# Optimization experiments

Hardware: AMD Instinct MI355X
Metric: run time of the kernel (lower is better)

Reference implementation:

```python
import jax, jax.numpy as jnp
import numpy as np

NUM_NODES = 50000
NUM_EDGES = 600000
NUM_FEAT = 128
HIDDEN = 512
N_OUT = 128
K = 3
N_GRAPHS = 128


def setup_inputs() -> dict:
    key = jax.random.key(0)
    ks = jax.random.split(key, 12)
    feature = jax.random.normal(ks[0], (NUM_NODES, NUM_FEAT), dtype=jnp.float32)
    edge_index = jax.random.randint(ks[1], (2, NUM_EDGES), 0, NUM_NODES, dtype=jnp.int64)
    protein_batch = jnp.sort(jax.random.randint(ks[2], (NUM_NODES,), 0, N_GRAPHS, dtype=jnp.int64))
    s = 0.05
    # ChebConv weights stored [K, in, out] (x @ W), single shared bias per conv
    W1 = jax.random.normal(ks[3], (K, NUM_FEAT, NUM_FEAT), dtype=jnp.float32) * s
    b1 = jax.random.normal(ks[4], (NUM_FEAT,), dtype=jnp.float32) * s
    W2 = jax.random.normal(ks[5], (K, NUM_FEAT, 2 * NUM_FEAT), dtype=jnp.float32) * s
    b2 = jax.random.normal(ks[6], (2 * NUM_FEAT,), dtype=jnp.float32) * s
    fc1_w = jax.random.normal(ks[7], (3 * NUM_FEAT, HIDDEN), dtype=jnp.float32) * s
    fc1_b = jax.random.normal(ks[8], (HIDDEN,), dtype=jnp.float32) * s
    fc2_w = jax.random.normal(ks[9], (HIDDEN, N_OUT), dtype=jnp.float32) * s
    fc2_b = jax.random.normal(ks[10], (N_OUT,), dtype=jnp.float32) * s
    return {"feature": feature, "edge_index": edge_index, "protein_batch": protein_batch,
            "W1": W1, "b1": b1, "W2": W2, "b2": b2,
            "fc1_w": fc1_w, "fc1_b": fc1_b, "fc2_w": fc2_w, "fc2_b": fc2_b}


def _cheb_conv(x, src, dst, edge_w, W, b):
    # PyG ChebConv with sym normalization, lambda_max=2 => scaled Laplacian
    # L_hat has zero diagonal and off-diag weights -1/sqrt(d_i d_j) (edge_w).
    def prop(h):
        return jax.ops.segment_sum(edge_w[:, None] * h[src], dst, num_segments=NUM_NODES)

    Tx0 = x
    out = Tx0 @ W[0]
    Tx1 = prop(x)
    out = out + Tx1 @ W[1]
    for k in range(2, W.shape[0]):
        Tx2 = 2.0 * prop(Tx1) - Tx0
        out = out + Tx2 @ W[k]
        Tx0, Tx1 = Tx1, Tx2
    return out + b


def reference(feature, edge_index, protein_batch, W1, b1, W2, b2, fc1_w, fc1_b, fc2_w, fc2_b):
    src, dst = edge_index[0], edge_index[1]
    deg = jax.ops.segment_sum(jnp.ones_like(src, dtype=feature.dtype), src, num_segments=NUM_NODES)
    dinv = jnp.where(deg > 0, jax.lax.rsqrt(jnp.maximum(deg, 1.0)), 0.0)
    edge_w = -dinv[src] * dinv[dst]  # (2/lambda_max)*L_sym off-diagonal; diag cancels to 0

    gx = jax.nn.relu(_cheb_conv(feature, src, dst, edge_w, W1, b1))
    gx = jax.nn.relu(_cheb_conv(gx, src, dst, edge_w, W2, b2))
    gx = jnp.concatenate([gx, feature], axis=1)  # [N, 3*F]

    # global_mean_pool
    sums = jax.ops.segment_sum(gx, protein_batch, num_segments=N_GRAPHS)
    cnts = jax.ops.segment_sum(jnp.ones((gx.shape[0],), gx.dtype), protein_batch, num_segments=N_GRAPHS)
    pooled = sums / jnp.maximum(cnts, 1.0)[:, None]

    h = jax.nn.relu(pooled @ fc1_w + fc1_b)  # dropout is identity in eval
    return h @ fc2_w + fc2_b
```

## Files before the change

kernel.cpp:

```cpp
#include <hip/hip_runtime.h>
#include <hip/hip_bf16.h>

#define NNODES 50000
#define NEDGES 600000
#define NB 196

typedef short vs8 __attribute__((ext_vector_type(8)));
typedef float floatx4 __attribute__((ext_vector_type(4)));

__device__ __forceinline__ float us2f(unsigned short u) {
    unsigned int x = ((unsigned int)u) << 16;
    float f;
    __builtin_memcpy(&f, &x, 4);
    return f;
}
__device__ __forceinline__ unsigned short f2us(float f) {
    unsigned int x;
    __builtin_memcpy(&x, &f, 4);
    unsigned int r = x + 0x7fffu + ((x >> 16) & 1u);
    return (unsigned short)(r >> 16);
}
__device__ __forceinline__ float ldf(const void* p, int i, int ff) {
    if (ff) return us2f(((const unsigned short*)p)[i]);
    return ((const float*)p)[i];
}
__device__ __forceinline__ int2 ldnt_sw(const int2* p) {
    unsigned long long v =
        __builtin_nontemporal_load(reinterpret_cast<const unsigned long long*>(p));
    int2 r;
    r.x = (int)(unsigned int)(v & 0xffffffffULL);
    r.y = (int)(unsigned int)(v >> 32);
    return r;
}

__global__ void k_detect(const int* ei, const unsigned int* fw, int* iflag, int* fflag) {
    int lane = threadIdx.x;
    int odd1 = ei[2 * lane + 1];
    int odd2 = ei[128 + 2 * lane + 1];
    unsigned long long nz = __ballot(odd1 != 0 || odd2 != 0);
    unsigned int e = (fw[lane] >> 7) & 0xffu;
    unsigned long long h = __ballot(e > 100u && e < 160u);
    if (lane == 0) {
        *iflag = (nz == 0ULL) ? 1 : 0;
        *fflag = (__popcll(h) > 40) ? 1 : 0;
    }
}

__global__ void k_init(const int* pb, const int* iflag, int* deg, int* indeg,
                       int* b32, float* psum) {
    int i = blockIdx.x * 256 + threadIdx.x;
    if (i < NNODES) {
        deg[i] = 0;
        indeg[i] = 0;
        int f = *iflag;
        b32[i] = pb[((size_t)i) << f];
    }
    if (i < 128 * 384) psum[i] = 0.f;
}

__global__ void k_degree(const int* ei, const int* iflag, int* deg, int* indeg,
                         int* rank) {
    int e = blockIdx.x * blockDim.x + threadIdx.x;
    if (e >= NEDGES) return;
    int f = *iflag;
    int s = ei[((size_t)e) << f];
    int d = ei[((size_t)(NEDGES + e)) << f];
    atomicAdd(&deg[s], 1);
    int r = atomicAdd(&indeg[d], 1);
    rank[e] = r;
}

__global__ void k_scan1(const int* indeg, const int* deg, int* bsum, float* dinv) {
    __shared__ int sh[256];
    int t = threadIdx.x;
    int i = blockIdx.x * 256 + t;
    int v = (i < NNODES) ? indeg[i] : 0;
    if (i < NNODES) {
        int d = deg[i];
        dinv[i] = d > 0 ? rsqrtf((float)d) : 0.f;
    }
    sh[t] = v;
    __syncthreads();
    for (int off = 128; off > 0; off >>= 1) {
        if (t < off) sh[t] += sh[t + off];
        __syncthreads();
    }
    if (t == 0) bsum[blockIdx.x] = sh[0];
}

__global__ void k_scan2(const int* bsum, int* boff, int* rowptr,
                        const int* batch32, int* pcnt) {
    __shared__ int sh[256];
    int t = threadIdx.x;
    int v = (t < NB) ? bsum[t] : 0;
    sh[t] = v;
    __syncthreads();
    for (int off = 1; off < 256; off <<= 1) {
        int x = (t >= off) ? sh[t - off] : 0;
        __syncthreads();
        sh[t] += x;
        __syncthreads();
    }
    if (t < NB) boff[t] = sh[t] - v;
    if (t == 255) rowptr[NNODES] = sh[255];
    if (t < 128) {
        int g = t;
        int lo = 0, hi = NNODES;
        while (lo < hi) { int mid = (lo + hi) >> 1; if (batch32[mid] < g) lo = mid + 1; else hi = mid; }
        int start = lo;
        hi = NNODES;
        while (lo < hi) { int mid = (lo + hi) >> 1; if (batch32[mid] <= g) lo = mid + 1; else hi = mid; }
        pcnt[g] = lo - start;
    }
}

__global__ void k_scan3(const int* indeg, const int* boff, int* rowptr) {
    __shared__ int sh[256];
    int t = threadIdx.x;
    int i = blockIdx.x * 256 + t;
    int v = (i < NNODES) ? indeg[i] : 0;
    sh[t] = v;
    __syncthreads();
    for (int off = 1; off < 256; off <<= 1) {
        int x = (t >= off) ? sh[t - off] : 0;
        __syncthreads();
        sh[t] += x;
        __syncthreads();
    }
    int excl = sh[t] - v + boff[blockIdx.x];
    if (i < NNODES) rowptr[i] = excl;
}

__global__ void k_fill(const int* ei, const int* iflag, const float* dinv,
                       const int* rowptr, const int* rank, int2* csr_sw) {
    int e = blockIdx.x * blockDim.x + threadIdx.x;
    if (e >= NEDGES) return;
    int f = *iflag;
    int s = ei[((size_t)e) << f];
    int d = ei[((size_t)(NEDGES + e)) << f];
    float w = -dinv[s] * dinv[d];
    int p = rowptr[d] + rank[e];
    int wb;
    __builtin_memcpy(&wb, &w, 4);
    int2 sw;
    sw.x = s;
    sw.y = wb;
    csr_sw[p] = sw;
}

__global__ void k_featb(const void* src, const int* fflag, unsigned short* dst) {
    int i = blockIdx.x * 256 + threadIdx.x;
    if (i >= NNODES * 128 / 8) return;
    if (*fflag) {
        reinterpret_cast<uint4*>(dst)[i] = reinterpret_cast<const uint4*>(src)[i];
    } else {
        const float4* fs = reinterpret_cast<const float4*>(src);
        float4 a = fs[2 * i], b = fs[2 * i + 1];
        uint4 o;
        o.x = (unsigned int)f2us(a.x) | ((unsigned int)f2us(a.y) << 16);
        o.y = (unsigned int)f2us(a.z) | ((unsigned int)f2us(a.w) << 16);
        o.z = (unsigned int)f2us(b.x) | ((unsigned int)f2us(b.y) << 16);
        o.w = (unsigned int)f2us(b.z) | ((unsigned int)f2us(b.w) << 16);
        reinterpret_cast<uint4*>(dst)[i] = o;
    }
}

__global__ void k_trans2(const void* W1, const void* W2, const int* fflag,
                         unsigned short* W1t, unsigned short* W2t) {
    int idx = blockIdx.x * 256 + threadIdx.x;
    int ff = *fflag;
    if (idx < 49152) {
        int n = idx / 384, k = idx - n * 384;
        float v;
        if (k < 128) v = ldf(W1, k * 128 + n, ff) - ldf(W1, (256 + k) * 128 + n, ff);
        else if (k < 256) v = ldf(W1, k * 128 + n, ff);
        else v = 2.f * ldf(W1, k * 128 + n, ff);
        W1t[idx] = f2us(v);
    } else if (idx < 49152 + 98304) {
        int j = idx - 49152;
        int n = j / 384, k = j - n * 384;
        float v;
        if (k < 128) v = ldf(W2, k * 256 + n, ff) - ldf(W2, (256 + k) * 256 + n, ff);
        else if (k < 256) v = ldf(W2, k * 256 + n, ff);
        else v = 2.f * ldf(W2, k * 256 + n, ff);
        W2t[j] = f2us(v);
    }
}

__global__ void k_prepw(const void* b1, const void* b2, const void* f1w, const void* f1b,
                        const void* f2w, const void* f2b, const int* fflag,
                        float* b1f, float* b2f, float* f1wf, float* f1bf,
                        float* f2wf, float* f2bf) {
    int i = blockIdx.x * 256 + threadIdx.x;
    int ff = *fflag;
    if (i < 196608) { f1wf[i] = ldf(f1w, i, ff); return; }
    i -= 196608;
    if (i < 65536) { f2wf[i] = ldf(f2w, i, ff); return; }
    i -= 65536;
    if (i < 512) { f1bf[i] = ldf(f1b, i, ff); return; }
    i -= 512;
    if (i < 256) { b2f[i] = ldf(b2, i, ff); return; }
    i -= 256;
    if (i < 128) { b1f[i] = ldf(b1, i, ff); return; }
    i -= 128;
    if (i < 128) f2bf[i] = ldf(f2b, i, ff);
}

__global__ void k_prop(const unsigned short* X, const int* rowptr, const int2* csr_sw,
                       unsigned short* out) {
    int wvid = (blockIdx.x * blockDim.x + threadIdx.x) >> 6;
    int lane = threadIdx.x & 63;
    int q = lane >> 4;
    int ln = lane & 15;
    int node = wvid * 4 + q;
    if (node >= NNODES) return;
    int fo = ln * 8;
    int beg = rowptr[node], end = rowptr[node + 1];
    float a0 = 0.f, a1 = 0.f, a2 = 0.f, a3 = 0.f;
    float a4 = 0.f, a5 = 0.f, a6 = 0.f, a7 = 0.f;
    int j = beg;
    for (; j + 4 <= end; j += 4) {
        int2 e0 = ldnt_sw(csr_sw + j);
        int2 e1 = ldnt_sw(csr_sw + j + 1);
        int2 e2 = ldnt_sw(csr_sw + j + 2);
        int2 e3 = ldnt_sw(csr_sw + j + 3);
        uint4 u0 = *reinterpret_cast<const uint4*>(X + (size_t)e0.x * 128 + fo);
        uint4 u1 = *reinterpret_cast<const uint4*>(X + (size_t)e1.x * 128 + fo);
        uint4 u2 = *reinterpret_cast<const uint4*>(X + (size_t)e2.x * 128 + fo);
        uint4 u3 = *reinterpret_cast<const uint4*>(X + (size_t)e3.x * 128 + fo);
        float w0, w1, w2, w3;
        __builtin_memcpy(&w0, &e0.y, 4);
        __builtin_memcpy(&w1, &e1.y, 4);
        __builtin_memcpy(&w2, &e2.y, 4);
        __builtin_memcpy(&w3, &e3.y, 4);
        a0 += w0 * us2f((unsigned short)(u0.x & 0xffffu)) + w1 * us2f((unsigned short)(u1.x & 0xffffu))
            + w2 * us2f((unsigned short)(u2.x & 0xffffu)) + w3 * us2f((unsigned short)(u3.x & 0xffffu));
        a1 += w0 * us2f((unsigned short)(u0.x >> 16)) + w1 * us2f((unsigned short)(u1.x >> 16))
            + w2 * us2f((unsigned short)(u2.x >> 16)) + w3 * us2f((unsigned short)(u3.x >> 16));
        a2 += w0 * us2f((unsigned short)(u0.y & 0xffffu)) + w1 * us2f((unsigned short)(u1.y & 0xffffu))
            + w2 * us2f((unsigned short)(u2.y & 0xffffu)) + w3 * us2f((unsigned short)(u3.y & 0xffffu));
        a3 += w0 * us2f((unsigned short)(u0.y >> 16)) + w1 * us2f((unsigned short)(u1.y >> 16))
            + w2 * us2f((unsigned short)(u2.y >> 16)) + w3 * us2f((unsigned short)(u3.y >> 16));
        a4 += w0 * us2f((unsigned short)(u0.z & 0xffffu)) + w1 * us2f((unsigned short)(u1.z & 0xffffu))
            + w2 * us2f((unsigned short)(u2.z & 0xffffu)) + w3 * us2f((unsigned short)(u3.z & 0xffffu));
        a5 += w0 * us2f((unsigned short)(u0.z >> 16)) + w1 * us2f((unsigned short)(u1.z >> 16))
            + w2 * us2f((unsigned short)(u2.z >> 16)) + w3 * us2f((unsigned short)(u3.z >> 16));
        a6 += w0 * us2f((unsigned short)(u0.w & 0xffffu)) + w1 * us2f((unsigned short)(u1.w & 0xffffu))
            + w2 * us2f((unsigned short)(u2.w & 0xffffu)) + w3 * us2f((unsigned short)(u3.w & 0xffffu));
        a7 += w0 * us2f((unsigned short)(u0.w >> 16)) + w1 * us2f((unsigned short)(u1.w >> 16))
            + w2 * us2f((unsigned short)(u2.w >> 16)) + w3 * us2f((unsigned short)(u3.w >> 16));
    }
    for (; j < end; ++j) {
        int2 e = ldnt_sw(csr_sw + j);
        float w;
        __builtin_memcpy(&w, &e.y, 4);
        uint4 u = *reinterpret_cast<const uint4*>(X + (size_t)e.x * 128 + fo);
        a0 += w * us2f((unsigned short)(u.x & 0xffffu));
        a1 += w * us2f((unsigned short)(u.x >> 16));
        a2 += w * us2f((unsigned short)(u.y & 0xffffu));
        a3 += w * us2f((unsigned short)(u.y >> 16));
        a4 += w * us2f((unsigned short)(u.z & 0xffffu));
        a5 += w * us2f((unsigned short)(u.z >> 16));
        a6 += w * us2f((unsigned short)(u.w & 0xffffu));
        a7 += w * us2f((unsigned short)(u.w >> 16));
    }
    uint4 ov;
    ov.x = (unsigned int)f2us(a0) | ((unsigned int)f2us(a1) << 16);
    ov.y = (unsigned int)f2us(a2) | ((unsigned int)f2us(a3) << 16);
    ov.z = (unsigned int)f2us(a4) | ((unsigned int)f2us(a5) << 16);
    ov.w = (unsigned int)f2us(a6) | ((unsigned int)f2us(a7) << 16);
    *reinterpret_cast<uint4*>(out + (size_t)node * 128 + fo) = ov;
}

template <int POOL>
__global__ __launch_bounds__(512) void k_convg(
    const unsigned short* seg0, const unsigned short* seg1, const unsigned short* seg2,
    const unsigned short* Wt, const float* bias, unsigned short* out,
    const int* batch32, float* psum, int nout, int nslab) {
    __shared__ unsigned short shb[24576];
    __shared__ float sh_ps[512];
    int tid = threadIdx.x;
    int bid = blockIdx.x;
    int grp = 8 * nslab;
    int main_blocks = 24 * grp;
    int r, slab;
    if (bid < main_blocks) {
        int g = bid / grp;
        int rem = bid - g * grp;
        slab = rem >> 3;
        r = g * 8 + (rem & 7);
    } else {
        int t = bid - main_blocks;
        r = 192 + (t & 3);
        slab = t >> 2;
    }
    int col0 = slab * 64;
    if (POOL) sh_ps[tid] = 0.f;
#pragma unroll
    for (int it = 0; it < 6; ++it) {
        int idx = tid + it * 512;
        int kkt = idx >> 6, ln = idx & 63;
        int kk = kkt >> 2, t = kkt & 3;
        int col = col0 + t * 16 + (ln & 15);
        int ko = kk * 32 + (ln >> 4) * 8;
        uint4 v = *reinterpret_cast<const uint4*>(Wt + (size_t)col * 384 + ko);
        *reinterpret_cast<uint4*>(shb + idx * 8) = v;
    }
    __syncthreads();
    int wv = tid >> 6, lane = tid & 63;
    int m = lane & 15, kq = lane >> 4;
    int row0 = r * 256 + wv * 32;
    int rr0 = row0 + m;
    int rr1 = row0 + 16 + m;
    if (rr0 >= NNODES) rr0 = NNODES - 1;
    if (rr1 >= NNODES) rr1 = NNODES - 1;
    floatx4 acc[2][4];
#pragma unroll
    for (int rI = 0; rI < 2; ++rI)
#pragma unroll
        for (int t = 0; t < 4; ++t) {
            acc[rI][t][0] = 0.f; acc[rI][t][1] = 0.f; acc[rI][t][2] = 0.f; acc[rI][t][3] = 0.f;
        }
    const unsigned short* segs[3];
    segs[0] = seg0; segs[1] = seg1; segs[2] = seg2;
#pragma unroll
    for (int kk = 0; kk < 12; ++kk) {
        int sgi = kk >> 2, k4 = kk & 3;
        const unsigned short* S = segs[sgi];
        int ko = k4 * 32 + kq * 8;
        vs8 a0 = *reinterpret_cast<const vs8*>(S + (size_t)rr0 * 128 + ko);
        vs8 a1 = *reinterpret_cast<const vs8*>(S + (size_t)rr1 * 128 + ko);
#pragma unroll
        for (int t = 0; t < 4; ++t) {
            vs8 b = *reinterpret_cast<const vs8*>(shb + ((kk * 4 + t) * 64 + lane) * 8);
            acc[0][t] = __builtin_amdgcn_mfma_f32_16x16x32_bf16(a0, b, acc[0][t], 0, 0, 0);
            acc[1][t] = __builtin_amdgcn_mfma_f32_16x16x32_bf16(a1, b, acc[1][t], 0, 0, 0);
        }
    }
    if (POOL == 0) {
#pragma unroll
        for (int rI = 0; rI < 2; ++rI) {
            int orow_base = row0 + rI * 16 + kq * 4;
#pragma unroll
            for (int t = 0; t < 4; ++t) {
                int col = col0 + t * 16 + m;
                float bv = bias[col];
#pragma unroll
                for (int i = 0; i < 4; ++i) {
                    int rw = orow_base + i;
                    if (rw < NNODES) {
                        float v = acc[rI][t][i] + bv;
                        v = v > 0.f ? v : 0.f;
                        out[(size_t)rw * nout + col] = f2us(v);
                    }
                }
            }
        }
    } else {
        int g0 = batch32[r * 256];
#pragma unroll
        for (int rI = 0; rI < 2; ++rI) {
            int orow_base = row0 + rI * 16 + kq * 4;
            int gid[4];
#pragma unroll
            for (int i = 0; i < 4; ++i) {
                int rw = orow_base + i;
                gid[i] = rw < NNODES ? batch32[rw] : -1;
            }
#pragma unroll
            for (int t = 0; t < 4; ++t) {
                int col = col0 + t * 16 + m;
                float bv = bias[col];
                float run = 0.f;
                int curg = -1;
#pragma unroll
                for (int i = 0; i < 4; ++i) {
                    int g = gid[i];
                    if (g < 0) break;
                    float v = acc[rI][t][i] + bv;
                    v = v > 0.f ? v : 0.f;
                    if (g != curg) {
                        if (curg >= 0) {
                            int gl = curg - g0;
                            if (gl >= 0 && gl < 8) atomicAdd(&sh_ps[gl * 64 + t * 16 + m], run);
                            else atomicAdd(&psum[curg * 384 + col], run);
                        }
                        curg = g;
                        run = 0.f;
                    }
                    run += v;
                }
                if (curg >= 0) {
                    int gl = curg - g0;
                    if (gl >= 0 && gl < 8) atomicAdd(&sh_ps[gl * 64 + t * 16 + m], run);
                    else atomicAdd(&psum[curg * 384 + col], run);
                }
            }
        }
        __syncthreads();
        int gl = tid >> 6, c = tid & 63;
        float v = sh_ps[tid];
        int gg = g0 + gl;
        if (v != 0.f && gg < 128) atomicAdd(&psum[(size_t)gg * 384 + col0 + c], v);
    }
}

__global__ void k_poolnodes(const unsigned short* featb, const int* batch32, float* psum) {
    int col = threadIdx.x & 127;
    int half = threadIdx.x >> 7;
    int nbeg = blockIdx.x * 128 + half * 64;
    if (nbeg >= NNODES) return;
    int nend = nbeg + 64;
    if (nend > NNODES) nend = NNODES;
    float run = 0.f;
    int curg = batch32[nbeg];
    for (int n = nbeg; n < nend; ++n) {
        int g = batch32[n];
        if (g != curg) {
            atomicAdd(&psum[curg * 384 + 256 + col], run);
            run = 0.f;
            curg = g;
        }
        run += us2f(featb[(size_t)n * 128 + col]);
    }
    atomicAdd(&psum[curg * 384 + 256 + col], run);
}

__global__ void k_fc1(const float* psum, const int* pcnt, const float* w,
                      const float* b, float* h) {
    int g = blockIdx.x, j = threadIdx.x * 2;
    int c = pcnt[g];
    float inv = 1.f / (float)(c > 0 ? c : 1);
    float a0 = 0.f, a1 = 0.f;
    for (int k = 0; k < 384; ++k) {
        float p = psum[g * 384 + k];
        a0 += p * w[k * 512 + j];
        a1 += p * w[k * 512 + j + 1];
    }
    a0 = a0 * inv + b[j];
    a1 = a1 * inv + b[j + 1];
    h[g * 512 + j] = a0 > 0.f ? a0 : 0.f;
    h[g * 512 + j + 1] = a1 > 0.f ? a1 : 0.f;
}

__global__ void ChebModel_74380243632480_kernel(const float* h, const float* w,
                                                const float* b, const int* fflag,
                                                void* out) {
    int g = blockIdx.x, j = threadIdx.x;
    float acc = 0.f;
    for (int k = 0; k < 512; ++k) acc += h[g * 512 + k] * w[k * 128 + j];
    acc += b[j];
    if (*fflag) ((unsigned short*)out)[g * 128 + j] = f2us(acc);
    else ((float*)out)[g * 128 + j] = acc;
}

extern "C" void kernel_launch(void* const* d_in, const int* in_sizes, int n_in,
                              void* d_out, int out_size, void* d_ws, size_t ws_size,
                              hipStream_t stream) {
    const void* feature = d_in[0];
    const int* edge_index = (const int*)d_in[1];
    const int* batch = (const int*)d_in[2];
    const void* W1 = d_in[3];
    const void* b1 = d_in[4];
    const void* W2 = d_in[5];
    const void* b2 = d_in[6];
    const void* fc1w = d_in[7];
    const void* fc1b = d_in[8];
    const void* fc2w = d_in[9];
    const void* fc2b = d_in[10];

    char* ws = (char*)d_ws;
    size_t off = 0;
    int* iflag = (int*)(ws + off); off += 256;
    int* fflag = (int*)(ws + off); off += 256;
    int* deg = (int*)(ws + off); off += ((size_t)NNODES * 4 + 255) & ~(size_t)255;
    int* indeg = (int*)(ws + off); off += ((size_t)NNODES * 4 + 255) & ~(size_t)255;
    int* rowptr = (int*)(ws + off); off += ((size_t)(NNODES + 1) * 4 + 255) & ~(size_t)255;
    float* dinv = (float*)(ws + off); off += ((size_t)NNODES * 4 + 255) & ~(size_t)255;
    int* batch32 = (int*)(ws + off); off += ((size_t)NNODES * 4 + 255) & ~(size_t)255;
    int* bsum = (int*)(ws + off); off += 1024;
    int* boff = (int*)(ws + off); off += 1024;
    int* rank = (int*)(ws + off); off += ((size_t)NEDGES * 4 + 255) & ~(size_t)255;
    int2* csr_sw = (int2*)(ws + off); off += ((size_t)NEDGES * 8 + 255) & ~(size_t)255;
    unsigned short* featb = (unsigned short*)(ws + off); off += ((size_t)NNODES * 128 * 2 + 255) & ~(size_t)255;
    unsigned short* T1 = (unsigned short*)(ws + off); off += ((size_t)NNODES * 128 * 2 + 255) & ~(size_t)255;
    unsigned short* T2 = (unsigned short*)(ws + off); off += ((size_t)NNODES * 128 * 2 + 255) & ~(size_t)255;
    unsigned short* gx1 = (unsigned short*)(ws + off); off += ((size_t)NNODES * 128 * 2 + 255) & ~(size_t)255;
    unsigned short* W1t = (unsigned short*)(ws + off); off += ((size_t)49152 * 2 + 255) & ~(size_t)255;
    unsigned short* W2t = (unsigned short*)(ws + off); off += ((size_t)98304 * 2 + 255) & ~(size_t)255;
    float* b1f = (float*)(ws + off); off += 1024;
    float* b2f = (float*)(ws + off); off += 1024;
    float* fc1wf = (float*)(ws + off); off += ((size_t)196608 * 4 + 255) & ~(size_t)255;
    float* fc1bf = (float*)(ws + off); off += 2048;
    float* fc2wf = (float*)(ws + off); off += ((size_t)65536 * 4 + 255) & ~(size_t)255;
    float* fc2bf = (float*)(ws + off); off += 1024;
    float* psum = (float*)(ws + off); off += ((size_t)128 * 384 * 4 + 255) & ~(size_t)255;
    int* pcnt = (int*)(ws + off); off += 1024;
    float* hbuf = (float*)(ws + off); off += ((size_t)128 * 512 * 4 + 255) & ~(size_t)255;

    k_detect<<<1, 64, 0, stream>>>(edge_index, (const unsigned int*)feature, iflag, fflag);
    k_init<<<(NNODES + 255) / 256, 256, 0, stream>>>(batch, iflag, deg, indeg, batch32, psum);
    k_degree<<<(NEDGES + 255) / 256, 256, 0, stream>>>(edge_index, iflag, deg, indeg, rank);
    k_scan1<<<NB, 256, 0, stream>>>(indeg, deg, bsum, dinv);
    k_scan2<<<1, 256, 0, stream>>>(bsum, boff, rowptr, batch32, pcnt);
    k_scan3<<<NB, 256, 0, stream>>>(indeg, boff, rowptr);
    k_fill<<<(NEDGES + 255) / 256, 256, 0, stream>>>(edge_index, iflag, dinv, rowptr, rank, csr_sw);

    k_featb<<<(NNODES * 128 / 8 + 255) / 256, 256, 0, stream>>>(feature, fflag, featb);
    k_trans2<<<(49152 + 98304 + 255) / 256, 256, 0, stream>>>(W1, W2, fflag, W1t, W2t);
    k_prepw<<<(263168 + 255) / 256, 256, 0, stream>>>(b1, b2, fc1w, fc1b, fc2w, fc2b, fflag,
                                                      b1f, b2f, fc1wf, fc1bf, fc2wf, fc2bf);

    int pb = ((NNODES + 3) / 4 * 64 + 255) / 256;
    k_prop<<<pb, 256, 0, stream>>>(featb, rowptr, csr_sw, T1);
    k_prop<<<pb, 256, 0, stream>>>(T1, rowptr, csr_sw, T2);
    k_convg<0><<<196 * 2, 512, 0, stream>>>(featb, T1, T2, W1t, b1f, gx1,
                                            (const int*)0, (float*)0, 128, 2);
    k_prop<<<pb, 256, 0, stream>>>(gx1, rowptr, csr_sw, T1);
    k_prop<<<pb, 256, 0, stream>>>(T1, rowptr, csr_sw, T2);
    k_convg<1><<<196 * 4, 512, 0, stream>>>(gx1, T1, T2, W2t, b2f, (unsigned short*)0,
                                            batch32, psum, 256, 4);
    k_poolnodes<<<(NNODES + 127) / 128, 256, 0, stream>>>(featb, batch32, psum);
    k_fc1<<<128, 256, 0, stream>>>(psum, pcnt, fc1wf, fc1bf, hbuf);
    ChebModel_74380243632480_kernel<<<128, 128, 0, stream>>>(hbuf, fc2wf, fc2bf, fflag, d_out);
}
```

Before: 410.4 us.

## Build CSR via two-level bucket sort and LDS degree histograms instead of global atomics

Replaces the global-atomic degree/rank computation and three-pass scan with per-block shared-memory histograms (degree packed two nodes per 32-bit word) and a two-level bucket sort over destination buckets of 256 nodes to build the CSR. The aim is to avoid contended global atomics and the separate rank array. Temporary buffers reuse T1/T2 workspace. The packing stores the source index in 16 bits (s | (d&255)<<16), but node ids reach 50000, so sources of 65536 or more would be corrupted; packed 16-bit degree counts could also overflow on skewed graphs.

```diff
diff --git a/kernel.cpp b/kernel.cpp
--- a/kernel.cpp
+++ b/kernel.cpp
@@ -4,6 +4,11 @@
 #define NNODES 50000
 #define NEDGES 600000
 #define NB 196
+#define NBKT 196
+#define SB 192
+#define SCH (NEDGES / SB)
+#define DEGB 64
+#define DEGCH (NEDGES / DEGB)
 
 typedef short vs8 __attribute__((ext_vector_type(8)));
 typedef float floatx4 __attribute__((ext_vector_type(4)));
@@ -46,63 +51,90 @@
     }
 }
 
-__global__ void k_init(const int* pb, const int* iflag, int* deg, int* indeg,
-                       int* b32, float* psum) {
+__global__ void k_init(const int* pb, const int* iflag, int* b32, float* psum) {
     int i = blockIdx.x * 256 + threadIdx.x;
     if (i < NNODES) {
-        deg[i] = 0;
-        indeg[i] = 0;
         int f = *iflag;
         b32[i] = pb[((size_t)i) << f];
     }
     if (i < 128 * 384) psum[i] = 0.f;
 }
 
-__global__ void k_degree(const int* ei, const int* iflag, int* deg, int* indeg,
-                         int* rank) {
-    int e = blockIdx.x * blockDim.x + threadIdx.x;
-    if (e >= NEDGES) return;
+__global__ __launch_bounds__(256) void k_deghist(const int* ei, const int* iflag,
+                                                 unsigned int* degpart) {
+    __shared__ unsigned int h[25000];
+    int t = threadIdx.x, blk = blockIdx.x;
+    for (int i = t; i < 25000; i += 256) h[i] = 0u;
+    __syncthreads();
     int f = *iflag;
-    int s = ei[((size_t)e) << f];
-    int d = ei[((size_t)(NEDGES + e)) << f];
-    atomicAdd(&deg[s], 1);
-    int r = atomicAdd(&indeg[d], 1);
-    rank[e] = r;
-}
-
-__global__ void k_scan1(const int* indeg, const int* deg, int* bsum, float* dinv) {
-    __shared__ int sh[256];
+    int e0 = blk * DEGCH;
+    for (int j = t; j < DEGCH; j += 256) {
+        int e = e0 + j;
+        int s = ei[((size_t)e) << f];
+        atomicAdd(&h[s >> 1], (s & 1) ? 65536u : 1u);
+    }
+    __syncthreads();
+    unsigned int* dp = degpart + (size_t)blk * 25000;
+    for (int i = t; i < 25000; i += 256) dp[i] = h[i];
+}
+
+__global__ void k_dred(const unsigned int* degpart, float* dinv) {
+    int i = blockIdx.x * 256 + threadIdx.x;
+    if (i >= 25000) return;
+    unsigned int lo = 0, hi = 0;
+    for (int b = 0; b < DEGB; ++b) {
+        unsigned int p = degpart[(size_t)b * 25000 + i];
+        lo += p & 0xffffu;
+        hi += p >> 16;
+    }
+    dinv[2 * i] = lo ? rsqrtf((float)lo) : 0.f;
+    dinv[2 * i + 1] = hi ? rsqrtf((float)hi) : 0.f;
+}
+
+__global__ void k_cnt(const int* ei, const int* iflag, int* cntpart) {
+    __shared__ int c[NBKT];
+    int t = threadIdx.x, blk = blockIdx.x;
+    if (t < NBKT) c[t] = 0;
+    __syncthreads();
+    int f = *iflag;
+    int e0 = blk * SCH;
+    for (int j = t; j < SCH; j += 256) {
+        int d = ei[((size_t)(NEDGES + e0 + j)) << f];
+        atomicAdd(&c[d >> 8], 1);
+    }
+    __syncthreads();
+    if (t < NBKT) cntpart[blk * NBKT + t] = c[t];
+}
+
+__global__ void k_bscan(const int* cntpart, int* bbase, int* gbase,
+                        const int* batch32, int* pcnt, int* rowptr) {
+    __shared__ int tot[256];
     int t = threadIdx.x;
-    int i = blockIdx.x * 256 + t;
-    int v = (i < NNODES) ? indeg[i] : 0;
-    if (i < NNODES) {
-        int d = deg[i];
-        dinv[i] = d > 0 ? rsqrtf((float)d) : 0.f;
-    }
-    sh[t] = v;
-    __syncthreads();
-    for (int off = 128; off > 0; off >>= 1) {
-        if (t < off) sh[t] += sh[t + off];
+    int sum = 0;
+    if (t < NBKT) {
+        for (int b = 0; b < SB; ++b) sum += cntpart[b * NBKT + t];
+    }
+    tot[t] = sum;
+    __syncthreads();
+    for (int off = 1; off < 256; off <<= 1) {
+        int x = (t >= off) ? tot[t - off] : 0;
         __syncthreads();
-    }
-    if (t == 0) bsum[blockIdx.x] = sh[0];
-}
-
-__global__ void k_scan2(const int* bsum, int* boff, int* rowptr,
-                        const int* batch32, int* pcnt) {
-    __shared__ int sh[256];
-    int t = threadIdx.x;
-    int v = (t < NB) ? bsum[t] : 0;
-    sh[t] = v;
-    __syncthreads();
-    for (int off = 1; off < 256; off <<= 1) {
-        int x = (t >= off) ? sh[t - off] : 0;
+        tot[t] += x;
         __syncthreads();
-        sh[t] += x;
-        __syncthreads();
-    }
-    if (t < NB) boff[t] = sh[t] - v;
-    if (t == 255) rowptr[NNODES] = sh[255];
+    }
+    int excl = tot[t] - sum;
+    if (t < NBKT) {
+        gbase[t] = excl;
+        int run = excl;
+        for (int b = 0; b < SB; ++b) {
+            bbase[b * NBKT + t] = run;
+            run += cntpart[b * NBKT + t];
+        }
+    }
+    if (t == 0) {
+        gbase[NBKT] = NEDGES;
+        rowptr[NNODES] = NEDGES;
+    }
     if (t < 128) {
         int g = t;
         int lo = 0, hi = NNODES;
@@ -114,38 +146,64 @@
     }
 }
 
-__global__ void k_scan3(const int* indeg, const int* boff, int* rowptr) {
-    __shared__ int sh[256];
-    int t = threadIdx.x;
-    int i = blockIdx.x * 256 + t;
-    int v = (i < NNODES) ? indeg[i] : 0;
-    sh[t] = v;
+__global__ void k_scat(const int* ei, const int* iflag, const float* dinv,
+                       const int* bbase, int2* bkt) {
+    __shared__ int cur[NBKT];
+    int t = threadIdx.x, blk = blockIdx.x;
+    if (t < NBKT) cur[t] = bbase[blk * NBKT + t];
+    __syncthreads();
+    int f = *iflag;
+    int e0 = blk * SCH;
+    for (int j = t; j < SCH; j += 256) {
+        int e = e0 + j;
+        int s = ei[((size_t)e) << f];
+        int d = ei[((size_t)(NEDGES + e)) << f];
+        float w = -dinv[s] * dinv[d];
+        int slot = atomicAdd(&cur[d >> 8], 1);
+        int wb;
+        __builtin_memcpy(&wb, &w, 4);
+        int2 v;
+        v.x = s | ((d & 255) << 16);
+        v.y = wb;
+        bkt[slot] = v;
+    }
+}
+
+__global__ void k_csr(const int2* bkt, const int* gbase, int* rowptr, int2* csr_sw) {
+    __shared__ int hist[256], scan[256], cur[256];
+    int t = threadIdx.x, b = blockIdx.x;
+    int beg = gbase[b], end = gbase[b + 1];
+    int n = end - beg;
+    hist[t] = 0;
+    __syncthreads();
+    for (int i = t; i < n; i += 256) {
+        int bin = (bkt[beg + i].x >> 16) & 255;
+        atomicAdd(&hist[bin], 1);
+    }
+    __syncthreads();
+    int h = hist[t];
+    scan[t] = h;
     __syncthreads();
     for (int off = 1; off < 256; off <<= 1) {
-        int x = (t >= off) ? sh[t - off] : 0;
+        int x = (t >= off) ? scan[t - off] : 0;
         __syncthreads();
-        sh[t] += x;
+        scan[t] += x;
         __syncthreads();
     }
-    int excl = sh[t] - v + boff[blockIdx.x];
-    if (i < NNODES) rowptr[i] = excl;
-}
-
-__global__ void k_fill(const int* ei, const int* iflag, const float* dinv,
-                       const int* rowptr, const int* rank, int2* csr_sw) {
-    int e = blockIdx.x * blockDim.x + threadIdx.x;
-    if (e >= NEDGES) return;
-    int f = *iflag;
-    int s = ei[((size_t)e) << f];
-    int d = ei[((size_t)(NEDGES + e)) << f];
-    float w = -dinv[s] * dinv[d];
-    int p = rowptr[d] + rank[e];
-    int wb;
-    __builtin_memcpy(&wb, &w, 4);
-    int2 sw;
-    sw.x = s;
-    sw.y = wb;
-    csr_sw[p] = sw;
+    int excl = scan[t] - h;
+    int node = b * 256 + t;
+    if (node < NNODES) rowptr[node] = beg + excl;
+    cur[t] = excl;
+    __syncthreads();
+    for (int i = t; i < n; i += 256) {
+        int2 p = bkt[beg + i];
+        int bin = (p.x >> 16) & 255;
+        int slot = atomicAdd(&cur[bin], 1);
+        int2 v;
+        v.x = p.x & 0xffff;
+        v.y = p.y;
+        csr_sw[beg + slot] = v;
+    }
 }
 
 __global__ void k_featb(const void* src, const int* fflag, unsigned short* dst) {
@@ -473,14 +531,12 @@
     size_t off = 0;
     int* iflag = (int*)(ws + off); off += 256;
     int* fflag = (int*)(ws + off); off += 256;
-    int* deg = (int*)(ws + off); off += ((size_t)NNODES * 4 + 255) & ~(size_t)255;
-    int* indeg = (int*)(ws + off); off += ((size_t)NNODES * 4 + 255) & ~(size_t)255;
     int* rowptr = (int*)(ws + off); off += ((size_t)(NNODES + 1) * 4 + 255) & ~(size_t)255;
     float* dinv = (float*)(ws + off); off += ((size_t)NNODES * 4 + 255) & ~(size_t)255;
     int* batch32 = (int*)(ws + off); off += ((size_t)NNODES * 4 + 255) & ~(size_t)255;
-    int* bsum = (int*)(ws + off); off += 1024;
-    int* boff = (int*)(ws + off); off += 1024;
-    int* rank = (int*)(ws + off); off += ((size_t)NEDGES * 4 + 255) & ~(size_t)255;
+    int* gbase = (int*)(ws + off); off += 1024;
+    int* cntpart = (int*)(ws + off); off += ((size_t)SB * NBKT * 4 + 255) & ~(size_t)255;
+    int* bbase = (int*)(ws + off); off += ((size_t)SB * NBKT * 4 + 255) & ~(size_t)255;
     int2* csr_sw = (int2*)(ws + off); off += ((size_t)NEDGES * 8 + 255) & ~(size_t)255;
     unsigned short* featb = (unsigned short*)(ws + off); off += ((size_t)NNODES * 128 * 2 + 255) & ~(size_t)255;
     unsigned short* T1 = (unsigned short*)(ws + off); off += ((size_t)NNODES * 128 * 2 + 255) & ~(size_t)255;
@@ -498,13 +554,17 @@
     int* pcnt = (int*)(ws + off); off += 1024;
     float* hbuf = (float*)(ws + off); off += ((size_t)128 * 512 * 4 + 255) & ~(size_t)255;
 
+    int2* bkt = (int2*)T1;
+    unsigned int* degpart = (unsigned int*)T2;
+
     k_detect<<<1, 64, 0, stream>>>(edge_index, (const unsigned int*)feature, iflag, fflag);
-    k_init<<<(NNODES + 255) / 256, 256, 0, stream>>>(batch, iflag, deg, indeg, batch32, psum);
-    k_degree<<<(NEDGES + 255) / 256, 256, 0, stream>>>(edge_index, iflag, deg, indeg, rank);
-    k_scan1<<<NB, 256, 0, stream>>>(indeg, deg, bsum, dinv);
-    k_scan2<<<1, 256, 0, stream>>>(bsum, boff, rowptr, batch32, pcnt);
-    k_scan3<<<NB, 256, 0, stream>>>(indeg, boff, rowptr);
-    k_fill<<<(NEDGES + 255) / 256, 256, 0, stream>>>(edge_index, iflag, dinv, rowptr, rank, csr_sw);
+    k_init<<<(NNODES + 255) / 256, 256, 0, stream>>>(batch, iflag, batch32, psum);
+    k_deghist<<<DEGB, 256, 0, stream>>>(edge_index, iflag, degpart);
+    k_dred<<<(25000 + 255) / 256, 256, 0, stream>>>(degpart, dinv);
+    k_cnt<<<SB, 256, 0, stream>>>(edge_index, iflag, cntpart);
+    k_bscan<<<1, 256, 0, stream>>>(cntpart, bbase, gbase, batch32, pcnt, rowptr);
+    k_scat<<<SB, 256, 0, stream>>>(edge_index, iflag, dinv, bbase, bkt);
+    k_csr<<<NBKT, 256, 0, stream>>>(bkt, gbase, rowptr, csr_sw);
 
     k_featb<<<(NNODES * 128 / 8 + 255) / 256, 256, 0, stream>>>(feature, fflag, featb);
     k_trans2<<<(49152 + 98304 + 255) / 256, 256, 0, stream>>>(W1, W2, fflag, W1t, W2t);
```

After: 412.9 us. Within noise of the previous version (+0.6%).
